# Kernel optimization log

Hardware: AMD Instinct MI355X
Metric: run time of the kernel (lower is better)

The kernel has to match this reference:

```python
import jax, jax.numpy as jnp
import numpy as np
from jax import lax
import math

B, C, H, W = 8, 512, 24, 24
L = H * W
D_STATE = 16
D_INNER = 2 * C
DT_RANK = C // 16
K = 4
SCALE = 1.0 / math.sqrt(C)


def layer_norm(x, g, b, eps=1e-5):
    m = x.mean(-1, keepdims=True)
    v = ((x - m) ** 2).mean(-1, keepdims=True)
    return (x - m) * lax.rsqrt(v + eps) * g + b


def selective_scan(u, delta, A, Bm, Cm, Ds):
    # u, delta: (B,K,d,L); Bm, Cm: (B,K,N,L); A: (K,d,N); Ds: (K,d)
    us = jnp.moveaxis(u, -1, 0)      # (L,B,K,d)
    dts = jnp.moveaxis(delta, -1, 0)
    Bs = jnp.moveaxis(Bm, -1, 0)     # (L,B,K,N)
    Cs = jnp.moveaxis(Cm, -1, 0)

    def step(h, inp):
        u_t, dt_t, B_t, C_t = inp
        dA = jnp.exp(dt_t[..., None] * A)                      # (B,K,d,N)
        dBu = (dt_t * u_t)[..., None] * B_t[:, :, None, :]     # (B,K,d,N)
        h = dA * h + dBu
        y = jnp.einsum('bkdn,bkn->bkd', h, C_t)
        return h, y

    h0 = jnp.zeros(u.shape[:3] + (A.shape[-1],), u.dtype)
    _, ys = lax.scan(step, h0, (us, dts, Bs, Cs))
    y = jnp.moveaxis(ys, 0, -1)                                # (B,K,d,L)
    return y + Ds[None, :, :, None] * u


def ss2d(x, in_proj_w, dwconv_w, dwconv_b, x_proj_w, dt_proj_w, dt_proj_b,
         A_logs, Ds, out_norm_g, out_norm_b, out_proj_w):
    # x: (B,H,W,C) channel-last
    xz = x @ in_proj_w.T                                       # (B,H,W,2*d_inner)
    xi, z = jnp.split(xz, 2, axis=-1)
    xc = xi.transpose(0, 3, 1, 2)                              # (B,d_inner,H,W)
    xc = lax.conv_general_dilated(xc, dwconv_w, (1, 1), 'SAME',
                                  feature_group_count=D_INNER,
                                  dimension_numbers=('NCHW', 'OIHW', 'NCHW'))
    xc = jax.nn.silu(xc + dwconv_b[None, :, None, None])
    x_hw = xc.reshape(B, D_INNER, L)
    x_wh = xc.transpose(0, 1, 3, 2).reshape(B, D_INNER, L)
    xs = jnp.stack([x_hw, x_wh, x_hw[..., ::-1], x_wh[..., ::-1]], axis=1)  # (B,4,d,L)
    x_dbl = jnp.einsum('bkdl,kcd->bkcl', xs, x_proj_w)
    dt, Bm, Cm = jnp.split(x_dbl, [DT_RANK, DT_RANK + D_STATE], axis=2)
    delta = jax.nn.softplus(jnp.einsum('bkrl,kdr->bkdl', dt, dt_proj_w)
                            + dt_proj_b[None, :, :, None])
    A = -jnp.exp(A_logs)
    ys = selective_scan(xs, delta, A, Bm, Cm, Ds)              # (B,4,d,L)
    y_wh = ys[:, 1].reshape(B, D_INNER, W, H).transpose(0, 1, 3, 2).reshape(B, D_INNER, L)
    y_whr = ys[:, 3, :, ::-1].reshape(B, D_INNER, W, H).transpose(0, 1, 3, 2).reshape(B, D_INNER, L)
    y = ys[:, 0] + ys[:, 2, :, ::-1] + y_wh + y_whr
    y = y.reshape(B, D_INNER, H, W).transpose(0, 2, 3, 1)      # (B,H,W,d_inner)
    y = layer_norm(y, out_norm_g, out_norm_b)
    y = y * jax.nn.silu(z)
    return y @ out_proj_w.T                                    # (B,H,W,C)


def setup_inputs():
    key = jax.random.key(0)
    ks = jax.random.split(key, 10)
    n = lambda k, sh, s=0.02: jax.random.normal(k, sh, dtype=jnp.float32) * s
    return {
        'x5': jax.random.normal(ks[0], (B, C, H, W), dtype=jnp.float32),
        'conv_w': n(ks[1], (C, C)),
        'conv_b': jnp.zeros((C,), jnp.float32),
        'ln1_g': jnp.ones((C,), jnp.float32),
        'ln1_b': jnp.zeros((C,), jnp.float32),
        'in_proj_w': n(ks[2], (2 * D_INNER, C)),
        'dwconv_w': n(ks[3], (D_INNER, 1, 3, 3), 0.1),
        'dwconv_b': jnp.zeros((D_INNER,), jnp.float32),
        'x_proj_w': n(ks[4], (K, DT_RANK + 2 * D_STATE, D_INNER)),
        'dt_proj_w': n(ks[5], (K, D_INNER, DT_RANK), 0.1),
        'dt_proj_b': n(ks[6], (K, D_INNER), 0.1),
        'A_logs': jnp.tile(jnp.log(jnp.arange(1, D_STATE + 1, dtype=jnp.float32))[None, None, :],
                           (K, D_INNER, 1)),
        'Ds': jnp.ones((K, D_INNER), jnp.float32),
        'out_norm_g': jnp.ones((D_INNER,), jnp.float32),
        'out_norm_b': jnp.zeros((D_INNER,), jnp.float32),
        'out_proj_w': n(ks[7], (C, D_INNER)),
    }


def reference(x5, conv_w, conv_b, ln1_g, ln1_b, in_proj_w, dwconv_w, dwconv_b,
              x_proj_w, dt_proj_w, dt_proj_b, A_logs, Ds, out_norm_g, out_norm_b,
              out_proj_w):
    # 1x1 conv + residual
    x5 = jnp.einsum('bchw,oc->bohw', x5, conv_w) + conv_b[None, :, None, None] + x5
    x0 = x5.transpose(0, 2, 3, 1)                              # (B,H,W,C)
    # VSSBlock: x + SS2D(LN(x)); called twice on same input with same weights -> identical
    x00 = x0 + ss2d(layer_norm(x0, ln1_g, ln1_b), in_proj_w, dwconv_w, dwconv_b,
                    x_proj_w, dt_proj_w, dt_proj_b, A_logs, Ds,
                    out_norm_g, out_norm_b, out_proj_w)
    xq = x00.transpose(0, 3, 1, 2).reshape(B, C, L)            # (B,C,L)
    xq_flat = xq.transpose(0, 2, 1).reshape(B * L, C)          # (B*L, C)
    xk_flat = xq.transpose(1, 0, 2).reshape(C, B * L)          # (C, B*L)
    xw = (xq_flat @ xk_flat) * SCALE                           # (B*L, B*L)
    xw = xw.reshape(B * L, B, L).max(-1).mean(-1).reshape(B, L)
    xw = jax.nn.softmax(xw, axis=-1)
    norm0 = x5 / jnp.maximum(jnp.linalg.norm(x5, axis=1, keepdims=True), 1e-12)
    xw = xw[:, None, :]                                        # (B,1,L)
    xw_max = xw.max(-1, keepdims=True)
    mask = (xw == xw_max).astype(x5.dtype).reshape(B, 1, H, W)  # winner-take-all
    seeds = (norm0 * mask).sum((2, 3))                         # (B,C)
    # correlation (eval branch: relu), seeds act as 1x1 conv weights
    cor = jax.nn.relu(jnp.einsum('bchw,oc->bohw', norm0, seeds)).mean(1).reshape(B, L)
    mn = cor.min(1, keepdims=True)
    mx = cor.max(1, keepdims=True)
    cormap = ((cor - mn) / (mx - mn + 1e-12)).reshape(B, 1, H, W)
    x51 = x5 * cormap
    proto1 = x51.mean((0, 2, 3), keepdims=True)                # (1,C,1,1)
    return (x5, proto1, x5 * proto1 + x51, mask)
```

## Files before the change

### kernel.cpp

```cpp
#include <hip/hip_runtime.h>
#include <math.h>

#define NB 8
#define NC 512
#define NH 24
#define NW 24
#define NL 576
#define ND 1024
#define NBL 4608
#define NCH 8
#define CL 72

static constexpr float SCALE_ = 0.044194173824159216f;

typedef __attribute__((ext_vector_type(8))) short bf16x8;
typedef __attribute__((ext_vector_type(4))) float f32x4;

__device__ __forceinline__ unsigned enc_f(float f){
    unsigned u = __float_as_uint(f);
    return (u & 0x80000000u) ? ~u : (u | 0x80000000u);
}
__device__ __forceinline__ float dec_f(unsigned e){
    return (e & 0x80000000u) ? __uint_as_float(e ^ 0x80000000u) : __uint_as_float(~e);
}

__device__ __forceinline__ int scan_idx(int t, int k){
    int t2 = (k >= 2) ? (NL - 1 - t) : t;
    return (k & 1) ? ((t2 % NH) * NW + t2 / NH) : t2;
}

__device__ __forceinline__ float softplus_f(float x){
    return fmaxf(x, 0.f) + __logf(1.f + __expf(-fabsf(x)));
}
__device__ __forceinline__ float silu_f(float x){
    return x / (1.f + __expf(-x));
}

__device__ __forceinline__ void split_bf(float v, unsigned short &h, unsigned short &l){
    unsigned u = __float_as_uint(v);
    unsigned hr = (u + 0x7fffu + ((u>>16)&1u)) >> 16;
    h = (unsigned short)hr;
    float hf = __uint_as_float(hr << 16);
    unsigned u2 = __float_as_uint(v - hf);
    l = (unsigned short)((u2 + 0x7fffu + ((u2>>16)&1u)) >> 16);
}

__global__ void k_transpose_in(const float* __restrict__ x5, float* __restrict__ x5t,
                               unsigned short* __restrict__ x5tB){
    __shared__ float t[32][33];
    const int b = blockIdx.z;
    const int c0 = blockIdx.x*32, l0 = blockIdx.y*32;
    const int tx = threadIdx.x & 31, ty = threadIdx.x >> 5;
    #pragma unroll
    for (int i=ty; i<32; i+=8)
        t[i][tx] = x5[((size_t)b*NC + c0 + i)*NL + l0 + tx];
    __syncthreads();
    #pragma unroll
    for (int i=ty; i<32; i+=8){
        float v = t[tx][i];
        x5t[((size_t)b*NL + l0 + i)*NC + c0 + tx] = v;
        unsigned short hh, ll; split_bf(v, hh, ll);
        size_t rb = ((size_t)b*NL + l0 + i)*1536 + c0 + tx;
        x5tB[rb] = hh; x5tB[rb+512] = ll; x5tB[rb+1024] = hh;
    }
}

template<int FORM>
__global__ void k_split(const float* __restrict__ in, unsigned short* __restrict__ oA,
                        unsigned short* __restrict__ oB, int K, int total4){
    int t = blockIdx.x*256 + threadIdx.x;
    if (t >= total4) return;
    int kq = K >> 2;
    int r = t / kq; int k4 = (t - r*kq) << 2;
    float4 v = *(const float4*)(in + (size_t)r*K + k4);
    float vv[4] = {v.x, v.y, v.z, v.w};
    unsigned short h[4], lo[4];
    #pragma unroll
    for (int i=0;i<4;i++) split_bf(vv[i], h[i], lo[i]);
    unsigned hp0 = h[0] | ((unsigned)h[1]<<16), hp1 = h[2] | ((unsigned)h[3]<<16);
    unsigned lp0 = lo[0] | ((unsigned)lo[1]<<16), lp1 = lo[2] | ((unsigned)lo[3]<<16);
    size_t base = (size_t)r*3*K + k4;
    if (FORM == 0 || FORM == 2){
        unsigned* p0 = (unsigned*)(oA + base);
        unsigned* p1 = (unsigned*)(oA + base + K);
        unsigned* p2 = (unsigned*)(oA + base + 2*K);
        p0[0]=hp0; p0[1]=hp1;  p1[0]=hp0; p1[1]=hp1;  p2[0]=lp0; p2[1]=lp1;
    }
    if (FORM == 1 || FORM == 2){
        unsigned short* o = (FORM==2) ? oB : oA;
        unsigned* p0 = (unsigned*)(o + base);
        unsigned* p1 = (unsigned*)(o + base + K);
        unsigned* p2 = (unsigned*)(o + base + 2*K);
        p0[0]=hp0; p0[1]=hp1;  p1[0]=lp0; p1[1]=lp1;  p2[0]=hp0; p2[1]=hp1;
    }
}

template<int MODE>
__launch_bounds__(256)
__global__ void mfma_nt(const unsigned short* __restrict__ A, const unsigned short* __restrict__ Bm,
                        const float* __restrict__ R0, const float* __restrict__ R1,
                        float* __restrict__ out0, float* __restrict__ out1,
                        unsigned* __restrict__ mbuf, int K3)
{
    const int bi = blockIdx.x, bj = blockIdx.y;
    if (MODE == 4 && bj < bi) return;
    const int m0 = bi*128, n0 = bj*128;
    __shared__ __align__(16) unsigned short As[128*32];
    __shared__ __align__(16) unsigned short Bs[128*32];
    const int tid = threadIdx.x;
    const int w = tid >> 6, l = tid & 63;
    const int mw = (w>>1)*64, nw = (w&1)*64;
    const int fr = l & 15, fq = l >> 4;

    f32x4 acc[4][4];
    #pragma unroll
    for (int i=0;i<4;i++)
        #pragma unroll
        for (int j=0;j<4;j++)
            #pragma unroll
            for (int c=0;c<4;c++) acc[i][j][c] = 0.f;

    const int c0 = tid, c1 = tid + 256;
    const int r0 = c0 >> 2, o0 = (c0 & 3) * 8;
    const int r1 = c1 >> 2, o1 = (c1 & 3) * 8;

    for (int k0 = 0; k0 < K3; k0 += 32){
        float4 a0 = *(const float4*)(A  + (size_t)(m0 + r0)*K3 + k0 + o0);
        float4 a1 = *(const float4*)(A  + (size_t)(m0 + r1)*K3 + k0 + o1);
        float4 b0 = *(const float4*)(Bm + (size_t)(n0 + r0)*K3 + k0 + o0);
        float4 b1 = *(const float4*)(Bm + (size_t)(n0 + r1)*K3 + k0 + o1);
        __syncthreads();
        *(float4*)&As[c0*8] = a0;
        *(float4*)&As[c1*8] = a1;
        *(float4*)&Bs[c0*8] = b0;
        *(float4*)&Bs[c1*8] = b1;
        __syncthreads();
        bf16x8 af[4], bf[4];
        #pragma unroll
        for (int i=0;i<4;i++){
            af[i] = *(const bf16x8*)&As[(mw + i*16 + fr)*32 + fq*8];
            bf[i] = *(const bf16x8*)&Bs[(nw + i*16 + fr)*32 + fq*8];
        }
        #pragma unroll
        for (int i=0;i<4;i++)
            #pragma unroll
            for (int j=0;j<4;j++)
                acc[i][j] = __builtin_amdgcn_mfma_f32_16x16x32_bf16(af[i], bf[j], acc[i][j], 0, 0, 0);
    }

    if (MODE == 4){
        const int b2c = (n0 + nw) / NL;
        #pragma unroll
        for (int mi=0; mi<4; mi++){
            #pragma unroll
            for (int i=0;i<4;i++){
                float v = fmaxf(fmaxf(acc[mi][0][i], acc[mi][1][i]),
                                fmaxf(acc[mi][2][i], acc[mi][3][i]));
                v = fmaxf(v, __shfl_xor(v, 1));
                v = fmaxf(v, __shfl_xor(v, 2));
                v = fmaxf(v, __shfl_xor(v, 4));
                v = fmaxf(v, __shfl_xor(v, 8));
                if (fr == 0)
                    atomicMax(&mbuf[(size_t)(m0 + mw + mi*16 + fq*4 + i)*NB + b2c], enc_f(v));
            }
        }
        const int b2r = (m0 + mw) / NL;
        #pragma unroll
        for (int ni=0; ni<4; ni++){
            float cm = -3.4e38f;
            #pragma unroll
            for (int mi=0; mi<4; mi++)
                #pragma unroll
                for (int i=0;i<4;i++) cm = fmaxf(cm, acc[mi][ni][i]);
            cm = fmaxf(cm, __shfl_xor(cm, 16));
            cm = fmaxf(cm, __shfl_xor(cm, 32));
            if (fq == 0)
                atomicMax(&mbuf[(size_t)(n0 + nw + ni*16 + fr)*NB + b2r], enc_f(cm));
        }
        return;
    }

    #pragma unroll
    for (int mi=0; mi<4; mi++){
        const int m = m0 + mw + mi*16 + fq*4;
        #pragma unroll
        for (int ni=0; ni<4; ni++){
            const int n = n0 + nw + ni*16 + fr;
            f32x4 a = acc[mi][ni];
            if (MODE == 0){
                float4 cb = *(const float4*)(R0 + m);
                float4 rs = *(const float4*)(R1 + (size_t)n*NC + m);
                float4 ov = make_float4(a[0]+cb.x+rs.x, a[1]+cb.y+rs.y, a[2]+cb.z+rs.z, a[3]+cb.w+rs.w);
                *(float4*)(out0 + (size_t)n*NC + m) = ov;
            } else if (MODE == 1){
                float4 ov = make_float4(a[0], a[1], a[2], a[3]);
                if (m < ND) *(float4*)(out0 + (size_t)n*ND + m) = ov;
                else        *(float4*)(out1 + (size_t)n*ND + (m - ND)) = ov;
            } else {
                float4 rs = *(const float4*)(R1 + (size_t)n*NC + m);
                float4 ov = make_float4(a[0]+rs.x, a[1]+rs.y, a[2]+rs.z, a[3]+rs.w);
                *(float4*)(out0 + (size_t)n*NC + m) = ov;
            }
        }
    }
}

template<int MODE>
__launch_bounds__(256)
__global__ void gemm_nt(const float* __restrict__ A0, const float* __restrict__ B0,
                        const float* __restrict__ R,
                        float* __restrict__ out0, float* __restrict__ out1,
                        unsigned* __restrict__ mbuf, int K)
{
    __shared__ __align__(16) float As[16][68];
    __shared__ __align__(16) float Bs[16][68];
    const int tid = threadIdx.x;
    const int m0 = blockIdx.x * 64;
    const int n0 = blockIdx.y * 64;
    const float* A = A0;
    const float* B = B0;
    int kdir = 0;
    if (MODE == 2) {
        const int bk = blockIdx.z;
        kdir = bk & 3; const int bb = bk >> 2;
        A = A0 + (size_t)kdir * 64 * 1024;
        B = B0 + (size_t)bb * NL * 1024;
    }
    const int lrow = tid >> 2;
    const int lk4  = (tid & 3) << 2;
    int brow = n0 + lrow;
    if (MODE == 2) brow = scan_idx(brow, kdir);
    const float* aptr = A + (size_t)(m0 + lrow) * K + lk4;
    const float* bptr = B + (size_t)brow * K + lk4;

    float acc[4][4];
    #pragma unroll
    for (int i=0;i<4;i++){
        #pragma unroll
        for (int j=0;j<4;j++) acc[i][j]=0.f;
    }
    const int tx = tid & 15, ty = tid >> 4;

    for (int k0 = 0; k0 < K; k0 += 16) {
        float4 av = *(const float4*)(aptr + k0);
        float4 bv = *(const float4*)(bptr + k0);
        __syncthreads();
        As[lk4+0][lrow]=av.x; As[lk4+1][lrow]=av.y; As[lk4+2][lrow]=av.z; As[lk4+3][lrow]=av.w;
        Bs[lk4+0][lrow]=bv.x; Bs[lk4+1][lrow]=bv.y; Bs[lk4+2][lrow]=bv.z; Bs[lk4+3][lrow]=bv.w;
        __syncthreads();
        #pragma unroll
        for (int kk=0;kk<16;kk++){
            float4 a = *(const float4*)&As[kk][ty<<2];
            float4 b = *(const float4*)&Bs[kk][tx<<2];
            acc[0][0] = fmaf(a.x,b.x,acc[0][0]); acc[0][1] = fmaf(a.x,b.y,acc[0][1]);
            acc[0][2] = fmaf(a.x,b.z,acc[0][2]); acc[0][3] = fmaf(a.x,b.w,acc[0][3]);
            acc[1][0] = fmaf(a.y,b.x,acc[1][0]); acc[1][1] = fmaf(a.y,b.y,acc[1][1]);
            acc[1][2] = fmaf(a.y,b.z,acc[1][2]); acc[1][3] = fmaf(a.y,b.w,acc[1][3]);
            acc[2][0] = fmaf(a.z,b.x,acc[2][0]); acc[2][1] = fmaf(a.z,b.y,acc[2][1]);
            acc[2][2] = fmaf(a.z,b.z,acc[2][2]); acc[2][3] = fmaf(a.z,b.w,acc[2][3]);
            acc[3][0] = fmaf(a.w,b.x,acc[3][0]); acc[3][1] = fmaf(a.w,b.y,acc[3][1]);
            acc[3][2] = fmaf(a.w,b.z,acc[3][2]); acc[3][3] = fmaf(a.w,b.w,acc[3][3]);
        }
    }

    #pragma unroll
    for (int j=0;j<4;j++){
        const int n  = n0 + (tx<<2) + j;
        const int mm = m0 + (ty<<2);
        float4 v = make_float4(acc[0][j], acc[1][j], acc[2][j], acc[3][j]);
        if (MODE == 2){
            *(float4*)(out0 + ((size_t)blockIdx.z*NL + n)*64 + mm) = v;
        }
    }
}

__global__ void k_ln512b(const float* __restrict__ x, const float* __restrict__ g,
                         const float* __restrict__ bb, unsigned short* __restrict__ outB){
    int n = blockIdx.x; int tid = threadIdx.x;
    const float* row = x + (size_t)n*NC;
    float v0 = row[tid], v1 = row[tid+256];
    __shared__ float s1[256], s2[256];
    s1[tid] = v0+v1; s2[tid] = v0*v0 + v1*v1;
    __syncthreads();
    for (int s=128;s>0;s>>=1){ if (tid<s){ s1[tid]+=s1[tid+s]; s2[tid]+=s2[tid+s]; } __syncthreads(); }
    float mean = s1[0]*(1.f/NC);
    float var  = fmaxf(s2[0]*(1.f/NC) - mean*mean, 0.f);
    float rs   = rsqrtf(var + 1e-5f);
    float r0 = (v0-mean)*rs*g[tid]     + bb[tid];
    float r1 = (v1-mean)*rs*g[tid+256] + bb[tid+256];
    unsigned short h0,l0,h1,l1; split_bf(r0,h0,l0); split_bf(r1,h1,l1);
    size_t base = (size_t)n*1536;
    outB[base+tid]     =h0; outB[base+512+tid]     =l0; outB[base+1024+tid]     =h0;
    outB[base+tid+256] =h1; outB[base+512+tid+256] =l1; outB[base+1024+tid+256] =h1;
}

__global__ void k_dwconv(const float* __restrict__ xi, const float* __restrict__ w,
                         const float* __restrict__ bias, float* __restrict__ xcl){
    int d = blockIdx.x*256 + threadIdx.x;
    int h = blockIdx.y; int b = blockIdx.z;
    float W[9];
    #pragma unroll
    for (int i=0;i<9;i++) W[i] = w[d*9+i];
    float bs = bias[d];
    const size_t rb = ((size_t)b*NL)*ND + d;
    const bool hm = h > 0, hp = h < NH-1;
    float p0=0.f,p1=0.f,p2=0.f;
    float c0 = hm ? xi[rb + (size_t)((h-1)*NW)*ND] : 0.f;
    float c1 = xi[rb + (size_t)(h*NW)*ND];
    float c2 = hp ? xi[rb + (size_t)((h+1)*NW)*ND] : 0.f;
    for (int wc=0; wc<NW; wc++){
        float n0,n1,n2;
        if (wc < NW-1){
            n0 = hm ? xi[rb + (size_t)((h-1)*NW+wc+1)*ND] : 0.f;
            n1 = xi[rb + (size_t)(h*NW+wc+1)*ND];
            n2 = hp ? xi[rb + (size_t)((h+1)*NW+wc+1)*ND] : 0.f;
        } else { n0=0.f;n1=0.f;n2=0.f; }
        float acc = bs;
        acc = fmaf(W[0],p0, fmaf(W[1],c0, fmaf(W[2],n0, acc)));
        acc = fmaf(W[3],p1, fmaf(W[4],c1, fmaf(W[5],n1, acc)));
        acc = fmaf(W[6],p2, fmaf(W[7],c2, fmaf(W[8],n2, acc)));
        xcl[rb + (size_t)(h*NW+wc)*ND] = silu_f(acc);
        p0=c0;p1=c1;p2=c2; c0=n0;c1=n1;c2=n2;
    }
}

#define DA_POWERS \
    float e1=__expf(-sp); float e2=e1*e1; float e3=e2*e1; float e4=e2*e2; \
    float e6=e4*e2; float e7=e4*e3; float e8=e4*e4; float e12=e8*e4; \
    float dA[16]; \
    dA[0]=e1; dA[1]=e2; dA[2]=e3; dA[3]=e4; dA[4]=e4*e1; dA[5]=e6; dA[6]=e7; dA[7]=e8; \
    dA[8]=e8*e1; dA[9]=e8*e2; dA[10]=e8*e3; dA[11]=e12; dA[12]=e12*e1; dA[13]=e12*e2; \
    dA[14]=e12*e3; dA[15]=e8*e8;

__launch_bounds__(256)
__global__ void k_scan_p1(const float* __restrict__ xcl, const float* __restrict__ xdbl,
                          const float* __restrict__ dtw, const float* __restrict__ dtb,
                          const float* __restrict__ alogs,
                          float* __restrict__ hfin, float* __restrict__ prodA){
    const int d = blockIdx.x*256 + threadIdx.x;
    const int chunk = blockIdx.y;
    const int bk = blockIdx.z;
    const int k = bk & 3, b = bk >> 2;
    const int kd = k*ND + d;
    float wdt[32];
    {
        const float4* p = (const float4*)(dtw + (size_t)kd*32);
        #pragma unroll
        for (int i=0;i<8;i++){ float4 v=p[i]; wdt[4*i]=v.x; wdt[4*i+1]=v.y; wdt[4*i+2]=v.z; wdt[4*i+3]=v.w; }
    }
    float An[16]; bool ladder = true;
    {
        const float4* p = (const float4*)(alogs + (size_t)kd*16);
        #pragma unroll
        for (int i=0;i<4;i++){
            float4 v=p[i];
            An[4*i]=-__expf(v.x); An[4*i+1]=-__expf(v.y); An[4*i+2]=-__expf(v.z); An[4*i+3]=-__expf(v.w);
        }
        #pragma unroll
        for (int n=0;n<16;n++) ladder = ladder && (fabsf(An[n] + (float)(n+1)) < 1e-3f*(n+1));
    }
    const float dtbias = dtb[kd];
    __shared__ __align__(16) float rows[CL*64];
    {
        const float4* src = (const float4*)(xdbl + ((size_t)bk*NL + chunk*CL)*64);
        for (int i = threadIdx.x; i < CL*16; i += 256) ((float4*)rows)[i] = src[i];
    }
    __syncthreads();
    float h[16], pA[16];
    #pragma unroll
    for (int n=0;n<16;n++){ h[n]=0.f; pA[n]=1.f; }
    if (ladder){
        for (int t=0;t<CL;t++){
            const float* row = rows + t*64;
            float dr = dtbias;
            #pragma unroll
            for (int r=0;r<32;r++) dr = fmaf(row[r], wdt[r], dr);
            float sp = softplus_f(dr);
            int idx = scan_idx(chunk*CL + t, k);
            float u  = xcl[((size_t)b*NL + idx)*ND + d];
            float du = sp * u;
            DA_POWERS
            #pragma unroll
            for (int n=0;n<16;n++){
                pA[n] *= dA[n];
                h[n] = fmaf(dA[n], h[n], du*row[32+n]);
            }
        }
    } else {
        for (int t=0;t<CL;t++){
            const float* row = rows + t*64;
            float dr = dtbias;
            #pragma unroll
            for (int r=0;r<32;r++) dr = fmaf(row[r], wdt[r], dr);
            float sp = softplus_f(dr);
            int idx = scan_idx(chunk*CL + t, k);
            float u  = xcl[((size_t)b*NL + idx)*ND + d];
            float du = sp * u;
            #pragma unroll
            for (int n=0;n<16;n++){
                float dA = __expf(sp * An[n]);
                pA[n] *= dA;
                h[n] = fmaf(dA, h[n], du*row[32+n]);
            }
        }
    }
    size_t base = (size_t)(bk*NCH + chunk)*16*1024 + d;
    #pragma unroll
    for (int n=0;n<16;n++){ hfin[base + n*1024] = h[n]; prodA[base + n*1024] = pA[n]; }
}

__global__ void k_scan_mid(float* __restrict__ hfin, const float* __restrict__ prodA){
    int id = blockIdx.x*256 + threadIdx.x;
    int d = id & 1023, nn = (id >> 10) & 15, bk = id >> 14;
    float h = 0.f;
    for (int j=0;j<NCH;j++){
        size_t idx = (size_t)((bk*NCH + j)*16 + nn)*1024 + d;
        float hf = hfin[idx], pa = prodA[idx];
        hfin[idx] = h;
        h = fmaf(pa, h, hf);
    }
}

__launch_bounds__(256)
__global__ void k_scan_p2(const float* __restrict__ xcl, const float* __restrict__ xdbl,
                          const float* __restrict__ dtw, const float* __restrict__ dtb,
                          const float* __restrict__ alogs,
                          const float* __restrict__ hfin, float* __restrict__ yacc){
    const int d = blockIdx.x*256 + threadIdx.x;
    const int chunk = blockIdx.y;
    const int bk = blockIdx.z;
    const int k = bk & 3, b = bk >> 2;
    const int kd = k*ND + d;
    float wdt[32];
    {
        const float4* p = (const float4*)(dtw + (size_t)kd*32);
        #pragma unroll
        for (int i=0;i<8;i++){ float4 v=p[i]; wdt[4*i]=v.x; wdt[4*i+1]=v.y; wdt[4*i+2]=v.z; wdt[4*i+3]=v.w; }
    }
    float An[16]; bool ladder = true;
    {
        const float4* p = (const float4*)(alogs + (size_t)kd*16);
        #pragma unroll
        for (int i=0;i<4;i++){
            float4 v=p[i];
            An[4*i]=-__expf(v.x); An[4*i+1]=-__expf(v.y); An[4*i+2]=-__expf(v.z); An[4*i+3]=-__expf(v.w);
        }
        #pragma unroll
        for (int n=0;n<16;n++) ladder = ladder && (fabsf(An[n] + (float)(n+1)) < 1e-3f*(n+1));
    }
    const float dtbias = dtb[kd];
    __shared__ __align__(16) float rows[CL*64];
    {
        const float4* src = (const float4*)(xdbl + ((size_t)bk*NL + chunk*CL)*64);
        for (int i = threadIdx.x; i < CL*16; i += 256) ((float4*)rows)[i] = src[i];
    }
    __syncthreads();
    float h[16];
    {
        size_t base = (size_t)(bk*NCH + chunk)*16*1024 + d;
        #pragma unroll
        for (int n=0;n<16;n++) h[n] = hfin[base + n*1024];
    }
    if (ladder){
        for (int t=0;t<CL;t++){
            const float* row = rows + t*64;
            float dr = dtbias;
            #pragma unroll
            for (int r=0;r<32;r++) dr = fmaf(row[r], wdt[r], dr);
            float sp = softplus_f(dr);
            int idx = scan_idx(chunk*CL + t, k);
            size_t base = ((size_t)b*NL + idx)*ND + d;
            float u  = xcl[base];
            float du = sp * u;
            float y = 0.f;
            DA_POWERS
            #pragma unroll
            for (int n=0;n<16;n++){
                h[n] = fmaf(dA[n], h[n], du*row[32+n]);
                y = fmaf(h[n], row[48+n], y);
            }
            atomicAdd(&yacc[base], y);
        }
    } else {
        for (int t=0;t<CL;t++){
            const float* row = rows + t*64;
            float dr = dtbias;
            #pragma unroll
            for (int r=0;r<32;r++) dr = fmaf(row[r], wdt[r], dr);
            float sp = softplus_f(dr);
            int idx = scan_idx(chunk*CL + t, k);
            size_t base = ((size_t)b*NL + idx)*ND + d;
            float u  = xcl[base];
            float du = sp * u;
            float y = 0.f;
            #pragma unroll
            for (int n=0;n<16;n++){
                float dA = __expf(sp * An[n]);
                h[n] = fmaf(dA, h[n], du*row[32+n]);
                y = fmaf(h[n], row[48+n], y);
            }
            atomicAdd(&yacc[base], y);
        }
    }
}

__global__ void k_combine(const float* __restrict__ y, const float* __restrict__ xcl,
                          const float* __restrict__ Ds,
                          const float* __restrict__ g, const float* __restrict__ bb,
                          const float* __restrict__ z, unsigned short* __restrict__ zB){
    int n = blockIdx.x;
    size_t base = (size_t)n*ND;
    int tid = threadIdx.x;
    float v[4]; float sum=0.f, sq=0.f;
    #pragma unroll
    for (int j=0;j<4;j++){
        int d = tid + 256*j;
        float ds = Ds[d] + Ds[ND+d] + Ds[2*ND+d] + Ds[3*ND+d];
        float val = y[base+d] + ds*xcl[base+d];
        v[j]=val; sum+=val; sq+=val*val;
    }
    __shared__ float s1[256], s2[256];
    s1[tid]=sum; s2[tid]=sq; __syncthreads();
    for (int st=128;st>0;st>>=1){ if(tid<st){ s1[tid]+=s1[tid+st]; s2[tid]+=s2[tid+st]; } __syncthreads(); }
    float mean = s1[0]*(1.f/ND);
    float var  = fmaxf(s2[0]*(1.f/ND) - mean*mean, 0.f);
    float rs   = rsqrtf(var + 1e-5f);
    size_t zb = (size_t)n*3072;
    #pragma unroll
    for (int j=0;j<4;j++){
        int d = tid + 256*j;
        float ln = (v[j]-mean)*rs*g[d] + bb[d];
        float res = ln * silu_f(z[base+d]);
        unsigned short hh,ll; split_bf(res,hh,ll);
        zB[zb + d] = hh; zB[zb + 1024 + d] = ll; zB[zb + 2048 + d] = hh;
    }
}

__global__ void k_xwpre(const unsigned* __restrict__ M, float* __restrict__ xwp){
    int n = blockIdx.x*256 + threadIdx.x; if (n >= NBL) return;
    float sum = 0.f;
    #pragma unroll
    for (int b2=0;b2<NB;b2++) sum += dec_f(M[(size_t)n*NB + b2]);
    xwp[n] = sum * (SCALE_/8.f);
}

__global__ void k_mask(const float* __restrict__ xwp, float* __restrict__ maskf){
    int b = blockIdx.x; int tid = threadIdx.x;
    float m = -1e30f;
    for (int i=tid;i<NL;i+=64) m = fmaxf(m, xwp[b*NL+i]);
    __shared__ float s1[64];
    s1[tid]=m; __syncthreads();
    for (int st=32;st>0;st>>=1){ if(tid<st) s1[tid]=fmaxf(s1[tid],s1[tid+st]); __syncthreads(); }
    float bm = s1[0];
    for (int i=tid;i<NL;i+=64) maskf[b*NL+i] = (xwp[b*NL+i]==bm) ? 1.f : 0.f;
}

__global__ void k_norm0(const float* __restrict__ x5r, float* __restrict__ norm0){
    int n = blockIdx.x; int tid = threadIdx.x;
    float v0 = x5r[(size_t)n*NC+tid], v1 = x5r[(size_t)n*NC+tid+256];
    __shared__ float s1[256];
    s1[tid] = v0*v0 + v1*v1; __syncthreads();
    for (int st=128;st>0;st>>=1){ if(tid<st) s1[tid]+=s1[tid+st]; __syncthreads(); }
    float inv = 1.f / fmaxf(sqrtf(s1[0]), 1e-12f);
    norm0[(size_t)n*NC+tid]     = v0*inv;
    norm0[(size_t)n*NC+tid+256] = v1*inv;
}

__global__ void k_seeds(const float* __restrict__ norm0, const float* __restrict__ maskf,
                        float* __restrict__ seeds){
    int b = blockIdx.x; int c = threadIdx.x;
    float acc = 0.f;
    for (int l=0;l<NL;l++){
        float mk = maskf[b*NL+l];
        if (mk != 0.f) acc += norm0[((size_t)b*NL+l)*NC + c]*mk;
    }
    seeds[b*NC + c] = acc;
}

__global__ void k_cor(const float* __restrict__ norm0, const float* __restrict__ seeds,
                      float* __restrict__ cor){
    int n = blockIdx.x; int tid = threadIdx.x;
    int o = tid >> 6, lane = tid & 63;
    float acc = 0.f;
    #pragma unroll
    for (int i=0;i<8;i++){
        int c = lane + 64*i;
        acc += norm0[(size_t)n*NC + c] * seeds[o*NC + c];
    }
    #pragma unroll
    for (int s=32;s>0;s>>=1) acc += __shfl_xor(acc, s);
    __shared__ float sr[8];
    if (lane == 0) sr[o] = fmaxf(acc, 0.f);
    __syncthreads();
    if (tid == 0){
        float r = 0.f;
        #pragma unroll
        for (int o2=0;o2<8;o2++) r += sr[o2];
        cor[n] = r * (1.f/8.f);
    }
}

__global__ void k_cormap(const float* __restrict__ cor, float* __restrict__ cmap){
    int b = blockIdx.x, tid = threadIdx.x;
    float mn = 1e30f, mx = -1e30f;
    for (int i=tid;i<NL;i+=64){ float v=cor[b*NL+i]; mn=fminf(mn,v); mx=fmaxf(mx,v); }
    __shared__ float sn[64], sx[64];
    sn[tid]=mn; sx[tid]=mx; __syncthreads();
    for (int st=32;st>0;st>>=1){ if(tid<st){ sn[tid]=fminf(sn[tid],sn[tid+st]); sx[tid]=fmaxf(sx[tid],sx[tid+st]); } __syncthreads(); }
    float MN=sn[0], MX=sx[0];
    float inv = 1.f/(MX-MN+1e-12f);
    for (int i=tid;i<NL;i+=64) cmap[b*NL+i] = (cor[b*NL+i]-MN)*inv;
}

__global__ void k_proto(const float* __restrict__ x5r, const float* __restrict__ cmap,
                        float* __restrict__ pacc){
    int c = threadIdx.x;
    int chunk = blockIdx.x;
    float acc = 0.f;
    for (int i=0;i<64;i++){
        int n = chunk*64 + i;
        acc += x5r[(size_t)n*NC + c] * cmap[n];
    }
    atomicAdd(&pacc[c], acc);
}

__global__ void k_final(const float* __restrict__ x5r, const float* __restrict__ cmap,
                        const float* __restrict__ pacc, const float* __restrict__ maskf,
                        float* __restrict__ out){
    int id = blockIdx.x*256 + threadIdx.x;
    int l = id % NL; int bc = id / NL; int c = bc & 511; int b = bc >> 9;
    float v  = x5r[((size_t)b*NL + l)*NC + c];
    float p  = pacc[c] * (1.f/(float)NBL);
    float cm = cmap[b*NL + l];
    out[id] = v;
    out[2359296 + 512 + id] = v*(p + cm);
    if (id < 512)  out[2359296 + id] = pacc[id] * (1.f/(float)NBL);
    if (id < NBL)  out[2359296 + 512 + 2359296 + id] = maskf[id];
}

extern "C" void kernel_launch(void* const* d_in, const int* in_sizes, int n_in,
                              void* d_out, int out_size, void* d_ws, size_t ws_size,
                              hipStream_t stream) {
    const float* x5        = (const float*)d_in[0];
    const float* conv_w    = (const float*)d_in[1];
    const float* conv_b    = (const float*)d_in[2];
    const float* ln1_g     = (const float*)d_in[3];
    const float* ln1_b     = (const float*)d_in[4];
    const float* in_proj_w = (const float*)d_in[5];
    const float* dwconv_w  = (const float*)d_in[6];
    const float* dwconv_b  = (const float*)d_in[7];
    const float* x_proj_w  = (const float*)d_in[8];
    const float* dt_proj_w = (const float*)d_in[9];
    const float* dt_proj_b = (const float*)d_in[10];
    const float* A_logs    = (const float*)d_in[11];
    const float* Ds        = (const float*)d_in[12];
    const float* out_norm_g= (const float*)d_in[13];
    const float* out_norm_b= (const float*)d_in[14];
    const float* out_proj_w= (const float*)d_in[15];

    float* ws = (float*)d_ws;
    const size_t O_X5R  = 0;
    const size_t O_XLN  = 2359296;
    const size_t O_XI   = 4718592;
    const size_t O_Z    = 9437184;
    const size_t O_XCL  = 14155776;
    const size_t O_XDBL = 18874368;
    const size_t O_HF   = 20054016;
    const size_t O_PA   = 24248320;
    const size_t O_MBUF = 28442624;
    const size_t O_XWP  = 28479488;
    const size_t O_MASK = 28484096;
    const size_t O_COR  = 28488704;
    const size_t O_CMAP = 28493312;
    const size_t O_SEED = 28497920;
    const size_t O_PACC = 28502016;

    float* x5r  = ws + O_X5R;
    float* xqf  = ws + O_XLN;
    float* xi   = ws + O_XI;
    float* yacc = ws + O_XI;
    unsigned short* wAo = (unsigned short*)(ws + O_XI);
    float* z    = ws + O_Z;
    float* xcl  = ws + O_XCL;
    unsigned short* wAi = (unsigned short*)(ws + O_XCL);
    float* nrm0 = ws + O_XCL;
    float* xdbl = ws + O_XDBL;
    float* x5t  = ws + O_HF;
    float* hfin = ws + O_HF;
    unsigned short* xlnB = (unsigned short*)(ws + O_HF);
    unsigned short* zB   = (unsigned short*)(ws + O_HF);
    unsigned short* xqfA = (unsigned short*)(ws + O_HF);
    float* prodA = ws + O_PA;
    unsigned short* x5tB = (unsigned short*)(ws + O_PA);
    unsigned short* wAc  = (unsigned short*)(ws + O_PA) + 7077888;
    unsigned short* xqfB = (unsigned short*)(ws + O_PA);
    unsigned* mbuf = (unsigned*)(ws + O_MBUF);
    float* xwp  = ws + O_XWP;
    float* maskf= ws + O_MASK;
    float* cor  = ws + O_COR;
    float* cmap = ws + O_CMAP;
    float* seeds= ws + O_SEED;
    float* pacc = ws + O_PACC;

    hipMemsetAsync(mbuf, 0, 36864*sizeof(unsigned), stream);
    hipMemsetAsync(pacc, 0, 512*sizeof(float), stream);

    k_transpose_in<<<dim3(16,18,8), 256, 0, stream>>>(x5, x5t, x5tB);
    k_split<0><<<256, 256, 0, stream>>>(conv_w, wAc, nullptr, 512, 65536);
    mfma_nt<0><<<dim3(4,36), 256, 0, stream>>>(wAc, x5tB, conv_b, x5t, x5r, nullptr, nullptr, 1536);
    k_ln512b<<<NBL, 256, 0, stream>>>(x5r, ln1_g, ln1_b, xlnB);
    k_split<0><<<1024, 256, 0, stream>>>(in_proj_w, wAi, nullptr, 512, 262144);
    mfma_nt<1><<<dim3(16,36), 256, 0, stream>>>(wAi, xlnB, nullptr, nullptr, xi, z, nullptr, 1536);
    k_dwconv<<<dim3(4,NH,NB), 256, 0, stream>>>(xi, dwconv_w, dwconv_b, xcl);
    hipMemsetAsync(yacc, 0, (size_t)4718592*sizeof(float), stream);
    gemm_nt<2><<<dim3(1,9,32), 256, 0, stream>>>(x_proj_w, xcl, nullptr, xdbl, nullptr, nullptr, 1024);
    k_scan_p1<<<dim3(4,NCH,32), 256, 0, stream>>>(xcl, xdbl, dt_proj_w, dt_proj_b, A_logs, hfin, prodA);
    k_scan_mid<<<2048, 256, 0, stream>>>(hfin, prodA);
    k_scan_p2<<<dim3(4,NCH,32), 256, 0, stream>>>(xcl, xdbl, dt_proj_w, dt_proj_b, A_logs, hfin, yacc);
    k_combine<<<NBL, 256, 0, stream>>>(yacc, xcl, Ds, out_norm_g, out_norm_b, z, zB);
    k_split<0><<<512, 256, 0, stream>>>(out_proj_w, wAo, nullptr, 1024, 131072);
    mfma_nt<3><<<dim3(4,36), 256, 0, stream>>>(wAo, zB, nullptr, x5r, xqf, nullptr, nullptr, 3072);
    k_split<2><<<2304, 256, 0, stream>>>(xqf, xqfA, xqfB, 512, 589824);
    mfma_nt<4><<<dim3(36,36), 256, 0, stream>>>(xqfA, xqfB, nullptr, nullptr, nullptr, nullptr, mbuf, 1536);
    k_xwpre<<<18, 256, 0, stream>>>(mbuf, xwp);
    k_mask<<<NB, 64, 0, stream>>>(xwp, maskf);
    k_norm0<<<NBL, 256, 0, stream>>>(x5r, nrm0);
    k_seeds<<<NB, 512, 0, stream>>>(nrm0, maskf, seeds);
    k_cor<<<NBL, 512, 0, stream>>>(nrm0, seeds, cor);
    k_cormap<<<NB, 64, 0, stream>>>(cor, cmap);
    k_proto<<<72, 512, 0, stream>>>(x5r, cmap, pacc);
    k_final<<<9216, 256, 0, stream>>>(x5r, cmap, pacc, maskf, (float*)d_out);
}
```

Baseline: 676.3 us.

## Prefetch GEMM tiles into registers, compact triangular grid, vectorize scan row reads

The MFMA GEMM now issues the global loads for the next K-tile right after the shared-memory store, so they overlap with the current tile's MFMAs. The symmetric MODE 4 launch maps a 1D grid of 666 blocks onto the upper triangle instead of launching 36x36 blocks and exiting the lower half early. The scan kernels read shared-memory rows as float4, split the dt dot product and the y reduction into independent partial sums to shorten dependency chains, and keep B/C in registers. The register prefetch raises register pressure, and the triangular index decode adds a small serial loop per block.

```diff
diff --git a/kernel.cpp b/kernel.cpp
--- a/kernel.cpp
+++ b/kernel.cpp
@@ -102,8 +102,12 @@
                         float* __restrict__ out0, float* __restrict__ out1,
                         unsigned* __restrict__ mbuf, int K3)
 {
-    const int bi = blockIdx.x, bj = blockIdx.y;
-    if (MODE == 4 && bj < bi) return;
+    int bi, bj;
+    if (MODE == 4){
+        int rem = blockIdx.x, len = 36; bi = 0;
+        while (rem >= len){ rem -= len; len--; bi++; }
+        bj = bi + rem;
+    } else { bi = blockIdx.x; bj = blockIdx.y; }
     const int m0 = bi*128, n0 = bj*128;
     __shared__ __align__(16) unsigned short As[128*32];
     __shared__ __align__(16) unsigned short Bs[128*32];
@@ -123,18 +127,29 @@
     const int c0 = tid, c1 = tid + 256;
     const int r0 = c0 >> 2, o0 = (c0 & 3) * 8;
     const int r1 = c1 >> 2, o1 = (c1 & 3) * 8;
+    const unsigned short* pA0 = A  + (size_t)(m0 + r0)*K3 + o0;
+    const unsigned short* pA1 = A  + (size_t)(m0 + r1)*K3 + o1;
+    const unsigned short* pB0 = Bm + (size_t)(n0 + r0)*K3 + o0;
+    const unsigned short* pB1 = Bm + (size_t)(n0 + r1)*K3 + o1;
+
+    float4 a0 = *(const float4*)(pA0);
+    float4 a1 = *(const float4*)(pA1);
+    float4 b0 = *(const float4*)(pB0);
+    float4 b1 = *(const float4*)(pB1);
 
     for (int k0 = 0; k0 < K3; k0 += 32){
-        float4 a0 = *(const float4*)(A  + (size_t)(m0 + r0)*K3 + k0 + o0);
-        float4 a1 = *(const float4*)(A  + (size_t)(m0 + r1)*K3 + k0 + o1);
-        float4 b0 = *(const float4*)(Bm + (size_t)(n0 + r0)*K3 + k0 + o0);
-        float4 b1 = *(const float4*)(Bm + (size_t)(n0 + r1)*K3 + k0 + o1);
         __syncthreads();
         *(float4*)&As[c0*8] = a0;
         *(float4*)&As[c1*8] = a1;
         *(float4*)&Bs[c0*8] = b0;
         *(float4*)&Bs[c1*8] = b1;
         __syncthreads();
+        if (k0 + 32 < K3){
+            a0 = *(const float4*)(pA0 + k0 + 32);
+            a1 = *(const float4*)(pA1 + k0 + 32);
+            b0 = *(const float4*)(pB0 + k0 + 32);
+            b1 = *(const float4*)(pB1 + k0 + 32);
+        }
         bf16x8 af[4], bf[4];
         #pragma unroll
         for (int i=0;i<4;i++){
@@ -325,12 +340,25 @@
 }
 
 #define DA_POWERS \
-    float e1=__expf(-sp); float e2=e1*e1; float e3=e2*e1; float e4=e2*e2; \
+    float e2=e1*e1; float e3=e2*e1; float e4=e2*e2; \
     float e6=e4*e2; float e7=e4*e3; float e8=e4*e4; float e12=e8*e4; \
     float dA[16]; \
     dA[0]=e1; dA[1]=e2; dA[2]=e3; dA[3]=e4; dA[4]=e4*e1; dA[5]=e6; dA[6]=e7; dA[7]=e8; \
     dA[8]=e8*e1; dA[9]=e8*e2; dA[10]=e8*e3; dA[11]=e12; dA[12]=e12*e1; dA[13]=e12*e2; \
     dA[14]=e12*e3; dA[15]=e8*e8;
+
+#define DOT4(rq, dtb, out) { \
+    float4 q0=rq[0],q1=rq[1],q2=rq[2],q3=rq[3],q4=rq[4],q5=rq[5],q6=rq[6],q7=rq[7]; \
+    float s0=0.f,s1=0.f,s2=0.f,s3=0.f; \
+    s0=fmaf(q0.x,wdt[0],s0);  s1=fmaf(q0.y,wdt[1],s1);  s2=fmaf(q0.z,wdt[2],s2);  s3=fmaf(q0.w,wdt[3],s3); \
+    s0=fmaf(q1.x,wdt[4],s0);  s1=fmaf(q1.y,wdt[5],s1);  s2=fmaf(q1.z,wdt[6],s2);  s3=fmaf(q1.w,wdt[7],s3); \
+    s0=fmaf(q2.x,wdt[8],s0);  s1=fmaf(q2.y,wdt[9],s1);  s2=fmaf(q2.z,wdt[10],s2); s3=fmaf(q2.w,wdt[11],s3); \
+    s0=fmaf(q3.x,wdt[12],s0); s1=fmaf(q3.y,wdt[13],s1); s2=fmaf(q3.z,wdt[14],s2); s3=fmaf(q3.w,wdt[15],s3); \
+    s0=fmaf(q4.x,wdt[16],s0); s1=fmaf(q4.y,wdt[17],s1); s2=fmaf(q4.z,wdt[18],s2); s3=fmaf(q4.w,wdt[19],s3); \
+    s0=fmaf(q5.x,wdt[20],s0); s1=fmaf(q5.y,wdt[21],s1); s2=fmaf(q5.z,wdt[22],s2); s3=fmaf(q5.w,wdt[23],s3); \
+    s0=fmaf(q6.x,wdt[24],s0); s1=fmaf(q6.y,wdt[25],s1); s2=fmaf(q6.z,wdt[26],s2); s3=fmaf(q6.w,wdt[27],s3); \
+    s0=fmaf(q7.x,wdt[28],s0); s1=fmaf(q7.y,wdt[29],s1); s2=fmaf(q7.z,wdt[30],s2); s3=fmaf(q7.w,wdt[31],s3); \
+    out = (s0+s1)+(s2+s3)+dtb; }
 
 __launch_bounds__(256)
 __global__ void k_scan_p1(const float* __restrict__ xcl, const float* __restrict__ xdbl,
@@ -371,31 +399,32 @@
     for (int n=0;n<16;n++){ h[n]=0.f; pA[n]=1.f; }
     if (ladder){
         for (int t=0;t<CL;t++){
-            const float* row = rows + t*64;
-            float dr = dtbias;
-            #pragma unroll
-            for (int r=0;r<32;r++) dr = fmaf(row[r], wdt[r], dr);
+            const float4* rq = (const float4*)(rows + t*64);
+            float dr; DOT4(rq, dtbias, dr);
             float sp = softplus_f(dr);
             int idx = scan_idx(chunk*CL + t, k);
             float u  = xcl[((size_t)b*NL + idx)*ND + d];
             float du = sp * u;
+            float e1 = __expf(-sp);
             DA_POWERS
+            float4 B0=rq[8],B1=rq[9],B2=rq[10],B3=rq[11];
+            const float Bv[16] = {B0.x,B0.y,B0.z,B0.w,B1.x,B1.y,B1.z,B1.w,
+                                  B2.x,B2.y,B2.z,B2.w,B3.x,B3.y,B3.z,B3.w};
             #pragma unroll
             for (int n=0;n<16;n++){
                 pA[n] *= dA[n];
-                h[n] = fmaf(dA[n], h[n], du*row[32+n]);
+                h[n] = fmaf(dA[n], h[n], du*Bv[n]);
             }
         }
     } else {
         for (int t=0;t<CL;t++){
-            const float* row = rows + t*64;
-            float dr = dtbias;
-            #pragma unroll
-            for (int r=0;r<32;r++) dr = fmaf(row[r], wdt[r], dr);
+            const float4* rq = (const float4*)(rows + t*64);
+            float dr; DOT4(rq, dtbias, dr);
             float sp = softplus_f(dr);
             int idx = scan_idx(chunk*CL + t, k);
             float u  = xcl[((size_t)b*NL + idx)*ND + d];
             float du = sp * u;
+            const float* row = rows + t*64;
             #pragma unroll
             for (int n=0;n<16;n++){
                 float dA = __expf(sp * An[n]);
@@ -463,35 +492,39 @@
     }
     if (ladder){
         for (int t=0;t<CL;t++){
-            const float* row = rows + t*64;
-            float dr = dtbias;
-            #pragma unroll
-            for (int r=0;r<32;r++) dr = fmaf(row[r], wdt[r], dr);
+            const float4* rq = (const float4*)(rows + t*64);
+            float dr; DOT4(rq, dtbias, dr);
             float sp = softplus_f(dr);
             int idx = scan_idx(chunk*CL + t, k);
             size_t base = ((size_t)b*NL + idx)*ND + d;
             float u  = xcl[base];
             float du = sp * u;
-            float y = 0.f;
+            float e1 = __expf(-sp);
             DA_POWERS
+            float4 B0=rq[8],B1=rq[9],B2=rq[10],B3=rq[11];
+            float4 C0=rq[12],C1=rq[13],C2=rq[14],C3=rq[15];
+            const float Bv[16] = {B0.x,B0.y,B0.z,B0.w,B1.x,B1.y,B1.z,B1.w,
+                                  B2.x,B2.y,B2.z,B2.w,B3.x,B3.y,B3.z,B3.w};
+            const float Cv[16] = {C0.x,C0.y,C0.z,C0.w,C1.x,C1.y,C1.z,C1.w,
+                                  C2.x,C2.y,C2.z,C2.w,C3.x,C3.y,C3.z,C3.w};
+            float y0=0.f, y1=0.f;
             #pragma unroll
             for (int n=0;n<16;n++){
-                h[n] = fmaf(dA[n], h[n], du*row[32+n]);
-                y = fmaf(h[n], row[48+n], y);
+                h[n] = fmaf(dA[n], h[n], du*Bv[n]);
+                if (n & 1) y1 = fmaf(h[n], Cv[n], y1); else y0 = fmaf(h[n], Cv[n], y0);
             }
-            atomicAdd(&yacc[base], y);
+            atomicAdd(&yacc[base], y0+y1);
         }
     } else {
         for (int t=0;t<CL;t++){
-            const float* row = rows + t*64;
-            float dr = dtbias;
-            #pragma unroll
-            for (int r=0;r<32;r++) dr = fmaf(row[r], wdt[r], dr);
+            const float4* rq = (const float4*)(rows + t*64);
+            float dr; DOT4(rq, dtbias, dr);
             float sp = softplus_f(dr);
             int idx = scan_idx(chunk*CL + t, k);
             size_t base = ((size_t)b*NL + idx)*ND + d;
             float u  = xcl[base];
             float du = sp * u;
+            const float* row = rows + t*64;
             float y = 0.f;
             #pragma unroll
             for (int n=0;n<16;n++){
@@ -721,7 +754,7 @@
     k_split<0><<<512, 256, 0, stream>>>(out_proj_w, wAo, nullptr, 1024, 131072);
     mfma_nt<3><<<dim3(4,36), 256, 0, stream>>>(wAo, zB, nullptr, x5r, xqf, nullptr, nullptr, 3072);
     k_split<2><<<2304, 256, 0, stream>>>(xqf, xqfA, xqfB, 512, 589824);
-    mfma_nt<4><<<dim3(36,36), 256, 0, stream>>>(xqfA, xqfB, nullptr, nullptr, nullptr, nullptr, mbuf, 1536);
+    mfma_nt<4><<<666, 256, 0, stream>>>(xqfA, xqfB, nullptr, nullptr, nullptr, nullptr, mbuf, 1536);
     k_xwpre<<<18, 256, 0, stream>>>(mbuf, xwp);
     k_mask<<<NB, 64, 0, stream>>>(xwp, maskf);
     k_norm0<<<NBL, 256, 0, stream>>>(x5r, nrm0);
```

After: 641.7 us. 1.05x faster.
